# Optimization experiments

Hardware: AMD Instinct MI355X
Metric: run time of the kernel (lower is better)

Reference implementation:

```python
import jax, jax.numpy as jnp
import numpy as np


def setup_inputs() -> dict:
    key = jax.random.key(0)
    kK, kP, ki, ke = jax.random.split(key, 4)
    B, n = 512, 4096
    K_batch = jax.random.normal(kK, (B, n), dtype=jnp.float32)
    # Phi must be symmetric PSD (the module treats it as a kernel/metric matrix:
    # grad of sum(R@A*R) is written as 2*R@A, valid only for symmetric A).
    W = jax.random.normal(kP, (n, n), dtype=jnp.float32) / np.float32(np.sqrt(n))
    Phi = W @ W.T  # eigenvalues O(1)
    imp = jax.random.normal(ki, (1024,), dtype=jnp.float32)
    exc = jax.random.normal(ke, (1024,), dtype=jnp.float32)
    a = jnp.float32(1.0)
    gamma = jnp.float32(1.0)
    return {"K_batch": K_batch, "a": a, "exc": exc, "imp": imp,
            "Phi": Phi, "gamma": gamma}


def reference(K_batch, a, exc, imp, Phi, gamma):
    """OptNet-style layer: solve, per sample i,
         min_r  (gamma/B)*||r||^2 + ((||imp||^2+||exc||^2)/B) * r^T Phi r
         s.t.   a * <r, k_i> = 1
    Closed-form KKT solution (what the original SPG iteration converges to):
         r_i = M^{-1} k_i / (a * k_i^T M^{-1} k_i),
         M   = (gamma/B) I + ((||imp||^2+||exc||^2)/B) Phi.
    """
    B, n = K_batch.shape
    imp2 = jnp.sum(imp * imp)   # ||imp||^2
    exc2 = jnp.sum(exc * exc)   # ||exc||^2
    M = (imp2 + exc2) / B * Phi + (gamma / B) * jnp.eye(n, dtype=K_batch.dtype)
    # z_i = M^{-1} k_i for all samples at once: solve with B right-hand sides.
    Z = jnp.linalg.solve(M, K_batch.T).T            # [B, n]
    denom = a * jnp.sum(Z * K_batch, axis=1)        # [B], = a * k_i^T M^{-1} k_i
    opt_x = Z / denom[:, None]                      # [B, n]
    return opt_x
```

## Files before the change

### kernel.cpp

```cpp
#include <hip/hip_runtime.h>


#define N    4096
#define NRHS 512
#define NB   128
#define PSTR 68
#define DSTR 136
#define TSTR 136
#define BSTR 36

__device__ __forceinline__ int xcd_map(int bid, int nwg) {
  int x = bid & 7, i = bid >> 3;
  int q = nwg >> 3, r = nwg & 7;
  return (x < r ? x * (q + 1) : r * (q + 1) + (x - r) * q) + i;
}

template<int S>
__device__ __forceinline__ void asm_levelA(float* __restrict__ sh, int tid) {
  constexpr int TOT = (64 / S) * S * (S / 4);
  constexpr int F4 = S / 4;
  for (int id = tid; id < TOT; id += 512) {
    int pair = id / (S * F4);
    int rem = id - pair * (S * F4);
    int r = rem / F4, c4 = rem - r * F4;
    int o = 2 * S * pair;
    const float* arow = &sh[(o + S + r) * DSTR + o];
    float4 a4 = {0.f, 0.f, 0.f, 0.f};
    for (int t = 0; t < S; ++t) {
      float a = arow[t];
      const float4 b = *(const float4*)&sh[(o + t) * DSTR + o + 4 * c4];
      a4.x += a * b.x; a4.y += a * b.y; a4.z += a * b.z; a4.w += a * b.w;
    }
    *(float4*)&sh[(S * pair + r) * DSTR + 64 + 4 * c4] = a4;
  }
}
template<int S>
__device__ __forceinline__ void asm_levelB(float* __restrict__ sh, int tid) {
  constexpr int TOT = (64 / S) * S * (S / 4);
  constexpr int F4 = S / 4;
  for (int id = tid; id < TOT; id += 512) {
    int pair = id / (S * F4);
    int rem = id - pair * (S * F4);
    int r = rem / F4, c4 = rem - r * F4;
    int o = 2 * S * pair;
    const float* u2row = &sh[(o + S + r) * DSTR + o + S];
    float4 a4 = {0.f, 0.f, 0.f, 0.f};
    for (int t = 0; t < S; ++t) {
      float a = u2row[t];
      const float4 w = *(const float4*)&sh[(S * pair + t) * DSTR + 64 + 4 * c4];
      a4.x += a * w.x; a4.y += a * w.y; a4.z += a * w.z; a4.w += a * w.w;
    }
    float4 ov = {-a4.x, -a4.y, -a4.z, -a4.w};
    *(float4*)&sh[(o + S + r) * DSTR + o + 4 * c4] = ov;
  }
}

__global__ __launch_bounds__(256) void k_scalars(const float* __restrict__ imp,
                                                 const float* __restrict__ exc,
                                                 const float* __restrict__ gamma,
                                                 float* __restrict__ c) {
  __shared__ float red[256];
  int tid = threadIdx.x;
  float s = 0.0f;
  for (int i = tid; i < 1024; i += 256) { float x = imp[i], y = exc[i]; s += x * x + y * y; }
  red[tid] = s; __syncthreads();
  for (int w = 128; w > 0; w >>= 1) { if (tid < w) red[tid] += red[tid + w]; __syncthreads(); }
  if (tid == 0) { c[0] = red[0] / 512.0f; c[1] = gamma[0] / 512.0f; }
}

__global__ __launch_bounds__(256) void k_build_M(const float* __restrict__ Phi,
                                                 const float* __restrict__ c,
                                                 float* __restrict__ M) {
  int idx = blockIdx.x * 256 + threadIdx.x;
  int base = idx * 4;
  float4 p = *(const float4*)(Phi + base);
  float c1 = c[0], c2 = c[1];
  float4 m;
  m.x = c1 * p.x; m.y = c1 * p.y; m.z = c1 * p.z; m.w = c1 * p.w;
  int r = base >> 12, c0 = base & (N - 1);
  if (r == c0)     m.x += c2;
  if (r == c0 + 1) m.y += c2;
  if (r == c0 + 2) m.z += c2;
  if (r == c0 + 3) m.w += c2;
  *(float4*)(M + base) = m;
}

__global__ __launch_bounds__(256) void k_transpose(const float* __restrict__ K,
                                                   float* __restrict__ S) {
  __shared__ float t[32][33];
  int bi = blockIdx.x, bb = blockIdx.y;
  int tx = threadIdx.x & 31, ty = threadIdx.x >> 5;
  for (int r = 0; r < 4; ++r)
    t[ty + 8 * r][tx] = K[(size_t)(bb * 32 + ty + 8 * r) * N + bi * 32 + tx];
  __syncthreads();
  for (int r = 0; r < 4; ++r)
    S[(size_t)(bi * 32 + ty + 8 * r) * NRHS + bb * 32 + tx] = t[tx][ty + 8 * r];
}

__global__ __launch_bounds__(512, 2) void k_syrk_potrf(float* __restrict__ M,
                                                       float* __restrict__ U,
                                                       int kdiag, int k0) {
  __shared__ float sh[NB * DSTR];
  __shared__ float dinv[NB];
  float* Pa = sh;
  float* Pb = sh + NB * PSTR;
  int tid = threadIdx.x;
  int p = (gridDim.x > 1) ? xcd_map(blockIdx.x, gridDim.x) : 0;
  int g4 = tid >> 4;
  int cm = tid & 15;
  int rr4 = g4 * 4;

  if (p > 0) {
    int br = (int)((sqrtf(8.f * (float)p + 1.f) - 1.f) * 0.5f);
    while (((br + 1) * (br + 2)) / 2 <= p) ++br;
    while ((br * (br + 1)) / 2 > p) --br;
    int bc = p - (br * (br + 1)) / 2;
    int t0k = kdiag * NB;
    int r0 = t0k + br * NB, c0 = t0k + bc * NB;
    float acc[4][8] = {};
    for (int ch = 0; ch < 2; ++ch) {
      int kc = k0 + ch * 64;
      __syncthreads();
#pragma unroll
      for (int i = 0; i < 4; ++i) {
        int idx = tid + (i << 9);
        int r = idx >> 4, f4 = idx & 15;
        *(float4*)&Pa[r * PSTR + 4 * f4] = *(const float4*)(M + (size_t)(r0 + r) * N + kc + 4 * f4);
        *(float4*)&Pb[r * PSTR + 4 * f4] = *(const float4*)(M + (size_t)(c0 + r) * N + kc + 4 * f4);
      }
      __syncthreads();
#pragma unroll 2
      for (int tc = 0; tc < 64; tc += 4) {
        float4 a4[4], b4[8];
#pragma unroll
        for (int q = 0; q < 4; ++q) a4[q] = *(const float4*)&Pa[(rr4 + ((q + g4) & 3)) * PSTR + tc];
#pragma unroll
        for (int w = 0; w < 8; ++w) b4[w] = *(const float4*)&Pb[(cm + 16 * w) * PSTR + tc];
#pragma unroll
        for (int q = 0; q < 4; ++q)
#pragma unroll
          for (int w = 0; w < 8; ++w)
            acc[q][w] += a4[q].x * b4[w].x + a4[q].y * b4[w].y
                       + a4[q].z * b4[w].z + a4[q].w * b4[w].w;
      }
    }
    for (int q = 0; q < 4; ++q) {
      int row = r0 + rr4 + ((q + g4) & 3);
      float* mp = M + (size_t)row * N + c0 + cm;
#pragma unroll
      for (int w = 0; w < 8; ++w) mp[16 * w] -= acc[q][w];
    }
    return;
  }

  int kr = kdiag * NB;
  float acc[4][8] = {};
  if (k0 >= 0) {
    for (int ch = 0; ch < 2; ++ch) {
      int kc = k0 + ch * 64;
      __syncthreads();
#pragma unroll
      for (int i = 0; i < 4; ++i) {
        int idx = tid + (i << 9);
        int r = idx >> 4, f4 = idx & 15;
        *(float4*)&Pa[r * PSTR + 4 * f4] = *(const float4*)(M + (size_t)(kr + r) * N + kc + 4 * f4);
      }
      __syncthreads();
#pragma unroll 2
      for (int tc = 0; tc < 64; tc += 4) {
        float4 a4[4], b4[8];
#pragma unroll
        for (int q = 0; q < 4; ++q) a4[q] = *(const float4*)&Pa[(rr4 + ((q + g4) & 3)) * PSTR + tc];
#pragma unroll
        for (int w = 0; w < 8; ++w) b4[w] = *(const float4*)&Pa[(cm + 16 * w) * PSTR + tc];
#pragma unroll
        for (int q = 0; q < 4; ++q)
#pragma unroll
          for (int w = 0; w < 8; ++w)
            acc[q][w] += a4[q].x * b4[w].x + a4[q].y * b4[w].y
                       + a4[q].z * b4[w].z + a4[q].w * b4[w].w;
      }
    }
  }
  __syncthreads();
#pragma unroll
  for (int e = 0; e < 8; ++e) {
    int idx = tid + (e << 9);
    int r = idx >> 5, f4 = idx & 31;
    *(float4*)&sh[r * DSTR + 4 * f4] = *(const float4*)(M + (size_t)(kr + r) * N + kr + 4 * f4);
  }
  __syncthreads();
#pragma unroll
  for (int q = 0; q < 4; ++q) {
    int row = rr4 + ((q + g4) & 3);
#pragma unroll
    for (int w = 0; w < 8; ++w) {
      int col = cm + 16 * w;
      if ((row >> 4) < (col >> 4)) sh[row * DSTR + col] = 0.0f;
      else if (k0 >= 0) sh[row * DSTR + col] -= acc[q][w];
    }
  }
  __syncthreads();

#pragma unroll 1
  for (int pp = 0; pp < 8; ++pp) {
    const int b0 = 16 * pp;
    if (tid < 16) {
      int l = tid;
      float r[16];
#pragma unroll
      for (int t = 0; t < 16; ++t) r[t] = sh[(b0 + l) * DSTR + b0 + t];
#pragma unroll
      for (int j = 0; j < 16; ++j) {
        float d = __shfl(r[j], j);
        float inv = rsqrtf(d);
        if (l == j) r[j] = d * inv;
        else if (l > j) r[j] *= inv;
        if (l == 0) dinv[b0 + j] = inv;
#pragma unroll
        for (int t = j + 1; t < 16; ++t) {
          float Ltj = __shfl(r[j], t);
          if (l >= t) r[t] -= r[j] * Ltj;
        }
      }
#pragma unroll
      for (int t = 0; t < 16; ++t) if (t <= l) sh[(b0 + l) * DSTR + b0 + t] = r[t];
    }
    __syncthreads();
    const int base = b0 + 16, nbl = NB - base;
    if (nbl > 0) {
      if (tid < nbl) {
        const int rg = base + tid;
        float xr[16];
#pragma unroll
        for (int j = 0; j < 16; ++j) {
          float v = sh[rg * DSTR + b0 + j];
#pragma unroll
          for (int t = 0; t < 16; ++t)
            if (t < j) v -= xr[t] * sh[(b0 + j) * DSTR + b0 + t];
          xr[j] = v * dinv[b0 + j];
          sh[rg * DSTR + b0 + j] = xr[j];
        }
      }
      __syncthreads();
      for (int i = tid >> 3; i < nbl; i += 64) {
        const float* ai = &sh[(base + i) * DSTR + b0];
        float4 a0 = *(const float4*)ai,       a1 = *(const float4*)(ai + 4);
        float4 a2 = *(const float4*)(ai + 8), a3 = *(const float4*)(ai + 12);
        for (int j = tid & 7; j <= i; j += 8) {
          const float* bj = &sh[(base + j) * DSTR + b0];
          float4 c0 = *(const float4*)bj,       c1 = *(const float4*)(bj + 4);
          float4 c2 = *(const float4*)(bj + 8), c3 = *(const float4*)(bj + 12);
          float s = a0.x*c0.x + a0.y*c0.y + a0.z*c0.z + a0.w*c0.w
                  + a1.x*c1.x + a1.y*c1.y + a1.z*c1.z + a1.w*c1.w
                  + a2.x*c2.x + a2.y*c2.y + a2.z*c2.z + a2.w*c2.w
                  + a3.x*c3.x + a3.y*c3.y + a3.z*c3.z + a3.w*c3.w;
          sh[(base + i) * DSTR + base + j] -= s;
        }
      }
      __syncthreads();
    }
  }

  if (tid < 128) {
    const int g = tid >> 4, l = tid & 15, b0 = 16 * g;
    float x[16];
#pragma unroll
    for (int i = 0; i < 16; ++i) {
      float s = (l == i) ? 1.0f : 0.0f;
#pragma unroll
      for (int t = 0; t < 16; ++t)
        if (t < i) s -= sh[(b0 + i) * DSTR + b0 + t] * x[t];
      x[i] = s * dinv[b0 + i];
      sh[(b0 + i) * DSTR + b0 + l] = x[i];
    }
  }
  __syncthreads();

  asm_levelA<16>(sh, tid); __syncthreads();
  asm_levelB<16>(sh, tid); __syncthreads();
  asm_levelA<32>(sh, tid); __syncthreads();
  asm_levelB<32>(sh, tid); __syncthreads();
  asm_levelA<64>(sh, tid); __syncthreads();
  asm_levelB<64>(sh, tid); __syncthreads();

#pragma unroll
  for (int e = 0; e < 8; ++e) {
    int idx = tid + (e << 9);
    int i = idx >> 5, f4 = idx & 31;
    float4 v;
    if ((i >> 4) >= (f4 >> 2)) v = *(const float4*)&sh[i * DSTR + 4 * f4];
    else v = make_float4(0.f, 0.f, 0.f, 0.f);
    *(float4*)(U + (size_t)i * NB + 4 * f4) = v;
  }
}

__global__ __launch_bounds__(512, 2) void k_trsm(float* __restrict__ M,
                                                 const float* __restrict__ Ug, int k0) {
  __shared__ float Pa[NB * PSTR];
  __shared__ float Pb[NB * PSTR];
  int tid = threadIdx.x;
  int g4 = tid >> 4, rr4 = g4 * 4, cm = tid & 15;
  int r0 = k0 + NB + blockIdx.x * NB;
  float acc[4][8] = {};
  for (int ch = 0; ch < 2; ++ch) {
    int kc = k0 + ch * 64;
    __syncthreads();
#pragma unroll
    for (int i = 0; i < 4; ++i) {
      int idx = tid + (i << 9);
      int r = idx >> 4, f4 = idx & 15;
      *(float4*)&Pa[r * PSTR + 4 * f4] = *(const float4*)(M + (size_t)(r0 + r) * N + kc + 4 * f4);
      *(float4*)&Pb[r * PSTR + 4 * f4] = *(const float4*)(Ug + (size_t)r * NB + ch * 64 + 4 * f4);
    }
    __syncthreads();
#pragma unroll 2
    for (int tc = 0; tc < 64; tc += 4) {
      float4 a4[4], b4[8];
#pragma unroll
      for (int q = 0; q < 4; ++q) a4[q] = *(const float4*)&Pa[(rr4 + ((q + g4) & 3)) * PSTR + tc];
#pragma unroll
      for (int w = 0; w < 8; ++w) b4[w] = *(const float4*)&Pb[(cm + 16 * w) * PSTR + tc];
#pragma unroll
      for (int q = 0; q < 4; ++q)
#pragma unroll
        for (int w = 0; w < 8; ++w)
          acc[q][w] += a4[q].x * b4[w].x + a4[q].y * b4[w].y
                     + a4[q].z * b4[w].z + a4[q].w * b4[w].w;
    }
  }
  for (int q = 0; q < 4; ++q) {
    int row = r0 + rr4 + ((q + g4) & 3);
    float* mp = M + (size_t)row * N + k0 + cm;
#pragma unroll
    for (int w = 0; w < 8; ++w) mp[16 * w] = acc[q][w];
  }
}

__global__ __launch_bounds__(256) void k_fsolve(float* __restrict__ S,
                                                float* __restrict__ X,
                                                const float* __restrict__ M,
                                                const float* __restrict__ Uk,
                                                int k0) {
  __shared__ float Xl[NB][BSTR];
  __shared__ float Aa[16][TSTR];
  __shared__ float Bb[16][BSTR];
  int tid = threadIdx.x;
  int id = xcd_map(blockIdx.x, gridDim.x);
  int d = id >> 4;
  int b0 = (id & 15) * 32;
  int i0g = k0 + d * NB;
  int ri = (tid & 31) * 4, ci = (tid >> 5) * 4;
  float acc[4][4] = {};
  for (int tch = 0; tch < NB; tch += 16) {
#pragma unroll
    for (int it = 0; it < 2; ++it) {
      int idx = tid + it * 256;
      int j = idx >> 2, f4 = idx & 3;
      const float4 v = *(const float4*)(Uk + (size_t)j * NB + tch + 4 * f4);
      Aa[4 * f4 + 0][j] = v.x; Aa[4 * f4 + 1][j] = v.y;
      Aa[4 * f4 + 2][j] = v.z; Aa[4 * f4 + 3][j] = v.w;
    }
    if (tid < 128) {
      int t = tid >> 3, f = tid & 7;
      *(float4*)&Bb[t][4 * f] = *(const float4*)(S + (size_t)(k0 + tch + t) * NRHS + b0 + 4 * f);
    }
    __syncthreads();
#pragma unroll 4
    for (int t = 0; t < 16; ++t) {
      float4 a = *(const float4*)&Aa[t][ri];
      float4 b = *(const float4*)&Bb[t][ci];
      float av[4] = {a.x, a.y, a.z, a.w};
      float bv[4] = {b.x, b.y, b.z, b.w};
#pragma unroll
      for (int q = 0; q < 4; ++q)
#pragma unroll
        for (int w = 0; w < 4; ++w) acc[q][w] += av[q] * bv[w];
    }
    __syncthreads();
  }
  if (d == 0) {
    for (int q = 0; q < 4; ++q) {
      float4 x0 = {acc[q][0], acc[q][1], acc[q][2], acc[q][3]};
      *(float4*)(X + (size_t)(k0 + ri + q) * NRHS + b0 + ci) = x0;
    }
    return;
  }
  for (int q = 0; q < 4; ++q) {
    float4 x0 = {acc[q][0], acc[q][1], acc[q][2], acc[q][3]};
    *(float4*)&Xl[ri + q][ci] = x0;
  }
  __syncthreads();
  float acc2[4][4] = {};
  for (int tch = 0; tch < NB; tch += 16) {
    for (int idx = tid; idx < 512; idx += 256) {
      int r = idx >> 2, q = idx & 3;
      const float4 v = *(const float4*)(M + (size_t)(i0g + r) * N + k0 + tch + 4 * q);
      Aa[4 * q + 0][r] = v.x; Aa[4 * q + 1][r] = v.y;
      Aa[4 * q + 2][r] = v.z; Aa[4 * q + 3][r] = v.w;
    }
    __syncthreads();
#pragma unroll 4
    for (int t = 0; t < 16; ++t) {
      float4 a = *(const float4*)&Aa[t][ri];
      float4 b = *(const float4*)&Xl[tch + t][ci];
      float av[4] = {a.x, a.y, a.z, a.w};
      float bv[4] = {b.x, b.y, b.z, b.w};
#pragma unroll
      for (int q = 0; q < 4; ++q)
#pragma unroll
        for (int w = 0; w < 4; ++w) acc2[q][w] += av[q] * bv[w];
    }
    __syncthreads();
  }
  for (int q = 0; q < 4; ++q) {
    float* sp = S + (size_t)(i0g + ri + q) * NRHS + b0 + ci;
    float4 x0 = *(float4*)sp;
    x0.x -= acc2[q][0]; x0.y -= acc2[q][1]; x0.z -= acc2[q][2]; x0.w -= acc2[q][3];
    *(float4*)sp = x0;
  }
}

__global__ __launch_bounds__(256) void k_bsolve(float* __restrict__ X,
                                                float* __restrict__ S,
                                                const float* __restrict__ M,
                                                const float* __restrict__ Uk,
                                                int k0) {
  __shared__ float Xl[NB][BSTR];
  __shared__ float Aa[16][TSTR];
  __shared__ float Bb[16][BSTR];
  int tid = threadIdx.x;
  int id = xcd_map(blockIdx.x, gridDim.x);
  int d = id >> 4;
  int b0 = (id & 15) * 32;
  int i0g = k0 - d * NB;
  int ri = (tid & 31) * 4, ci = (tid >> 5) * 4;
  float acc[4][4] = {};
  for (int tch = 0; tch < NB; tch += 16) {
    for (int idx = tid; idx < 512; idx += 256) {
      int t = idx >> 5, f = idx & 31;
      *(float4*)&Aa[t][4 * f] = *(const float4*)(Uk + (size_t)(tch + t) * NB + 4 * f);
    }
    if (tid < 128) {
      int t = tid >> 3, f = tid & 7;
      *(float4*)&Bb[t][4 * f] = *(const float4*)(X + (size_t)(k0 + tch + t) * NRHS + b0 + 4 * f);
    }
    __syncthreads();
#pragma unroll 4
    for (int t = 0; t < 16; ++t) {
      float4 a = *(const float4*)&Aa[t][ri];
      float4 b = *(const float4*)&Bb[t][ci];
      float av[4] = {a.x, a.y, a.z, a.w};
      float bv[4] = {b.x, b.y, b.z, b.w};
#pragma unroll
      for (int q = 0; q < 4; ++q)
#pragma unroll
        for (int w = 0; w < 4; ++w) acc[q][w] += av[q] * bv[w];
    }
    __syncthreads();
  }
  if (d == 0) {
    for (int q = 0; q < 4; ++q) {
      float4 x0 = {acc[q][0], acc[q][1], acc[q][2], acc[q][3]};
      *(float4*)(S + (size_t)(k0 + ri + q) * NRHS + b0 + ci) = x0;
    }
    return;
  }
  for (int q = 0; q < 4; ++q) {
    float4 x0 = {acc[q][0], acc[q][1], acc[q][2], acc[q][3]};
    *(float4*)&Xl[ri + q][ci] = x0;
  }
  __syncthreads();
  float acc2[4][4] = {};
  for (int tch = 0; tch < NB; tch += 16) {
    for (int idx = tid; idx < 512; idx += 256) {
      int t = idx >> 5, f = idx & 31;
      *(float4*)&Aa[t][4 * f] = *(const float4*)(M + (size_t)(k0 + tch + t) * N + i0g + 4 * f);
    }
    __syncthreads();
#pragma unroll 4
    for (int t = 0; t < 16; ++t) {
      float4 a = *(const float4*)&Aa[t][ri];
      float4 b = *(const float4*)&Xl[tch + t][ci];
      float av[4] = {a.x, a.y, a.z, a.w};
      float bv[4] = {b.x, b.y, b.z, b.w};
#pragma unroll
      for (int q = 0; q < 4; ++q)
#pragma unroll
        for (int w = 0; w < 4; ++w) acc2[q][w] += av[q] * bv[w];
    }
    __syncthreads();
  }
  for (int q = 0; q < 4; ++q) {
    float* xp = X + (size_t)(i0g + ri + q) * NRHS + b0 + ci;
    float4 x0 = *(float4*)xp;
    x0.x -= acc2[q][0]; x0.y -= acc2[q][1]; x0.z -= acc2[q][2]; x0.w -= acc2[q][3];
    *(float4*)xp = x0;
  }
}

__global__ __launch_bounds__(256) void k_final(const float* __restrict__ S,
                                               const float* __restrict__ K,
                                               const float* __restrict__ a_ptr,
                                               float* __restrict__ out) {
  __shared__ float red[256];
  int b = blockIdx.x, tid = threadIdx.x;
  float s = 0.0f;
  for (int i = tid; i < N; i += 256) s += S[(size_t)i * NRHS + b] * K[(size_t)b * N + i];
  red[tid] = s; __syncthreads();
  for (int w = 128; w > 0; w >>= 1) { if (tid < w) red[tid] += red[tid + w]; __syncthreads(); }
  float inv = 1.0f / (a_ptr[0] * red[0]);
  for (int i = tid; i < N; i += 256) out[(size_t)b * N + i] = S[(size_t)i * NRHS + b] * inv;
}

extern "C" void kernel_launch(void* const* d_in, const int* in_sizes, int n_in,
                              void* d_out, int out_size, void* d_ws, size_t ws_size,
                              hipStream_t stream) {
  const float* Kb    = (const float*)d_in[0];
  const float* a     = (const float*)d_in[1];
  const float* exc   = (const float*)d_in[2];
  const float* imp   = (const float*)d_in[3];
  const float* Phi   = (const float*)d_in[4];
  const float* gamma = (const float*)d_in[5];
  float* out = (float*)d_out;

  float* M  = (float*)d_ws;
  float* S  = M + (size_t)N * N;
  float* X  = S + (size_t)N * NRHS;
  float* U  = X + (size_t)N * NRHS;
  float* c  = U + (size_t)32 * NB * NB;

  k_scalars<<<1, 256, 0, stream>>>(imp, exc, gamma, c);
  k_build_M<<<N * N / 1024, 256, 0, stream>>>(Phi, c, M);
  k_transpose<<<dim3(N / 32, NRHS / 32), 256, 0, stream>>>(Kb, S);

  k_syrk_potrf<<<1, 512, 0, stream>>>(M, U, 0, -1);
  for (int k = 0; k <= 30; ++k) {
    int k0 = k * NB;
    k_trsm<<<31 - k, 512, 0, stream>>>(M, U + (size_t)k * NB * NB, k0);
    int T = 31 - k;
    int pairs = (T * (T + 1)) / 2;
    k_syrk_potrf<<<pairs, 512, 0, stream>>>(M, U + (size_t)(k + 1) * NB * NB, k + 1, k0);
  }
  for (int k = 0; k < 32; ++k)
    k_fsolve<<<16 * (32 - k), 256, 0, stream>>>(S, X, M, U + (size_t)k * NB * NB, k * NB);
  for (int k = 31; k >= 0; --k)
    k_bsolve<<<16 * (k + 1), 256, 0, stream>>>(X, S, M, U + (size_t)k * NB * NB, k * NB);
  k_final<<<NRHS, 256, 0, stream>>>(S, Kb, a, out);
}
```

Measured before the change: 4.688 ms.

## Overlap next diagonal block factorization with trailing update in panel Cholesky

The in-block Cholesky loop is restructured as a lookahead. The next 16x16 diagonal block gets its rank-16 update first, from 256 threads with one element each. Then one wave factors and inverts that corner while the remaining threads update the rest of the trailing matrix at the same time. Computing the triangular inverse inside the corner routine, using shuffles and the stored upper triangle, turns the later diagonal-inverse pass into a simple transpose copy. This shortens the serial critical path of the panel factorization, at the cost of more complex indexing and an extra barrier per step.

```diff
diff --git a/kernel.cpp b/kernel.cpp
--- a/kernel.cpp
+++ b/kernel.cpp
@@ -55,6 +55,42 @@
   }
 }
 
+__device__ __forceinline__ void corner_factor_inv(float* __restrict__ sh,
+                                                  float* __restrict__ dinv,
+                                                  int b0, int l) {
+  float r[16], invv[16];
+#pragma unroll
+  for (int t = 0; t < 16; ++t) r[t] = sh[(b0 + l) * DSTR + b0 + t];
+#pragma unroll
+  for (int j = 0; j < 16; ++j) {
+    float d = __shfl(r[j], j);
+    float inv = rsqrtf(d);
+    invv[j] = inv;
+    if (l == j) r[j] = d * inv;
+    else if (l > j) r[j] *= inv;
+    if (l == 0) dinv[b0 + j] = inv;
+#pragma unroll
+    for (int t = j + 1; t < 16; ++t) {
+      float Ltj = __shfl(r[j], t);
+      if (l >= t) r[t] -= r[j] * Ltj;
+    }
+  }
+#pragma unroll
+  for (int t = 0; t < 16; ++t) if (t <= l) sh[(b0 + l) * DSTR + b0 + t] = r[t];
+  float x[16];
+#pragma unroll
+  for (int i = 0; i < 16; ++i) {
+    float s = (l == i) ? 1.0f : 0.0f;
+#pragma unroll
+    for (int t = 0; t < 16; ++t)
+      if (t < i) s -= __shfl(r[t], i) * x[t];
+    x[i] = s * invv[i];
+  }
+#pragma unroll
+  for (int i = 0; i < 16; ++i)
+    if (i > l) sh[(b0 + l) * DSTR + b0 + i] = x[i];
+}
+
 __global__ __launch_bounds__(256) void k_scalars(const float* __restrict__ imp,
                                                  const float* __restrict__ exc,
                                                  const float* __restrict__ gamma,
@@ -202,78 +238,78 @@
   }
   __syncthreads();
 
+  if (tid < 16) corner_factor_inv(sh, dinv, 0, tid);
+  __syncthreads();
 #pragma unroll 1
-  for (int pp = 0; pp < 8; ++pp) {
+  for (int pp = 0; pp < 7; ++pp) {
     const int b0 = 16 * pp;
-    if (tid < 16) {
-      int l = tid;
-      float r[16];
-#pragma unroll
-      for (int t = 0; t < 16; ++t) r[t] = sh[(b0 + l) * DSTR + b0 + t];
+    const int base = b0 + 16, nbl = NB - base;
+    if (tid < nbl) {
+      const int rg = base + tid;
+      float xr[16];
 #pragma unroll
       for (int j = 0; j < 16; ++j) {
-        float d = __shfl(r[j], j);
-        float inv = rsqrtf(d);
-        if (l == j) r[j] = d * inv;
-        else if (l > j) r[j] *= inv;
-        if (l == 0) dinv[b0 + j] = inv;
-#pragma unroll
-        for (int t = j + 1; t < 16; ++t) {
-          float Ltj = __shfl(r[j], t);
-          if (l >= t) r[t] -= r[j] * Ltj;
-        }
-      }
-#pragma unroll
-      for (int t = 0; t < 16; ++t) if (t <= l) sh[(b0 + l) * DSTR + b0 + t] = r[t];
-    }
-    __syncthreads();
-    const int base = b0 + 16, nbl = NB - base;
-    if (nbl > 0) {
-      if (tid < nbl) {
-        const int rg = base + tid;
-        float xr[16];
-#pragma unroll
-        for (int j = 0; j < 16; ++j) {
-          float v = sh[rg * DSTR + b0 + j];
-#pragma unroll
-          for (int t = 0; t < 16; ++t)
-            if (t < j) v -= xr[t] * sh[(b0 + j) * DSTR + b0 + t];
-          xr[j] = v * dinv[b0 + j];
-          sh[rg * DSTR + b0 + j] = xr[j];
-        }
-      }
-      __syncthreads();
-      for (int i = tid >> 3; i < nbl; i += 64) {
-        const float* ai = &sh[(base + i) * DSTR + b0];
+        float v = sh[rg * DSTR + b0 + j];
+#pragma unroll
+        for (int t = 0; t < 16; ++t)
+          if (t < j) v -= xr[t] * sh[(b0 + j) * DSTR + b0 + t];
+        xr[j] = v * dinv[b0 + j];
+        sh[rg * DSTR + b0 + j] = xr[j];
+      }
+    }
+    __syncthreads();
+    if (tid < 256) {
+      int i = base + (tid >> 4), j = base + (tid & 15);
+      if (j <= i) {
+        const float* ai = &sh[i * DSTR + b0];
+        const float* bj = &sh[j * DSTR + b0];
         float4 a0 = *(const float4*)ai,       a1 = *(const float4*)(ai + 4);
         float4 a2 = *(const float4*)(ai + 8), a3 = *(const float4*)(ai + 12);
-        for (int j = tid & 7; j <= i; j += 8) {
-          const float* bj = &sh[(base + j) * DSTR + b0];
-          float4 c0 = *(const float4*)bj,       c1 = *(const float4*)(bj + 4);
-          float4 c2 = *(const float4*)(bj + 8), c3 = *(const float4*)(bj + 12);
-          float s = a0.x*c0.x + a0.y*c0.y + a0.z*c0.z + a0.w*c0.w
-                  + a1.x*c1.x + a1.y*c1.y + a1.z*c1.z + a1.w*c1.w
-                  + a2.x*c2.x + a2.y*c2.y + a2.z*c2.z + a2.w*c2.w
-                  + a3.x*c3.x + a3.y*c3.y + a3.z*c3.z + a3.w*c3.w;
-          sh[(base + i) * DSTR + base + j] -= s;
+        float4 c0 = *(const float4*)bj,       c1 = *(const float4*)(bj + 4);
+        float4 c2 = *(const float4*)(bj + 8), c3 = *(const float4*)(bj + 12);
+        float s = a0.x*c0.x + a0.y*c0.y + a0.z*c0.z + a0.w*c0.w
+                + a1.x*c1.x + a1.y*c1.y + a1.z*c1.z + a1.w*c1.w
+                + a2.x*c2.x + a2.y*c2.y + a2.z*c2.z + a2.w*c2.w
+                + a3.x*c3.x + a3.y*c3.y + a3.z*c3.z + a3.w*c3.w;
+        sh[i * DSTR + j] -= s;
+      }
+    }
+    __syncthreads();
+    if (tid < 16) {
+      corner_factor_inv(sh, dinv, base, tid);
+    } else if (tid >= 64) {
+      const int base2 = base + 16;
+      const int nb2 = NB - base2;
+      if (nb2 > 0) {
+        for (int i = base2 + ((tid - 64) >> 3); i < NB; i += 56) {
+          const float* ai = &sh[i * DSTR + b0];
+          float4 a0 = *(const float4*)ai,       a1 = *(const float4*)(ai + 4);
+          float4 a2 = *(const float4*)(ai + 8), a3 = *(const float4*)(ai + 12);
+          for (int j = base + (tid & 7); j <= i; j += 8) {
+            const float* bj = &sh[j * DSTR + b0];
+            float4 c0 = *(const float4*)bj,       c1 = *(const float4*)(bj + 4);
+            float4 c2 = *(const float4*)(bj + 8), c3 = *(const float4*)(bj + 12);
+            float s = a0.x*c0.x + a0.y*c0.y + a0.z*c0.z + a0.w*c0.w
+                    + a1.x*c1.x + a1.y*c1.y + a1.z*c1.z + a1.w*c1.w
+                    + a2.x*c2.x + a2.y*c2.y + a2.z*c2.z + a2.w*c2.w
+                    + a3.x*c3.x + a3.y*c3.y + a3.z*c3.z + a3.w*c3.w;
+            sh[i * DSTR + j] -= s;
+          }
         }
       }
-      __syncthreads();
-    }
+    }
+    __syncthreads();
   }
 
   if (tid < 128) {
     const int g = tid >> 4, l = tid & 15, b0 = 16 * g;
-    float x[16];
-#pragma unroll
-    for (int i = 0; i < 16; ++i) {
-      float s = (l == i) ? 1.0f : 0.0f;
-#pragma unroll
-      for (int t = 0; t < 16; ++t)
-        if (t < i) s -= sh[(b0 + i) * DSTR + b0 + t] * x[t];
-      x[i] = s * dinv[b0 + i];
-      sh[(b0 + i) * DSTR + b0 + l] = x[i];
-    }
+    float v[16];
+#pragma unroll
+    for (int i = 0; i < 16; ++i)
+      v[i] = (i > l) ? sh[(b0 + l) * DSTR + b0 + i] : ((i == l) ? dinv[b0 + l] : 0.0f);
+#pragma unroll
+    for (int i = 0; i < 16; ++i)
+      sh[(b0 + i) * DSTR + b0 + l] = v[i];
   }
   __syncthreads();
 
```

New measurement: 4.502 ms. -4.0%, faster.
